# Performance work log

Measured on AMD Instinct MI355X. Metric: run time of the kernel, lower is better.

The kernel has to match this reference:

```python
import jax, jax.numpy as jnp
import numpy as np

N, E = 50000, 600000
IN_C, HID, OUT_C = 256, 128, 2
R, B, L = 7, 8, 3
ALPHA = 0.1


def _rgcn(x, src, dst, etype, comp, basis, root, bias):
    # comp: [R,B], basis: [B,d,d] -> per-relation weights W: [R,d,d]
    n, d = x.shape
    W = jnp.einsum('rb,bdf->rdf', comp, basis)
    # combined (dst, relation) segment id for per-relation mean aggregation
    seg = dst * R + etype
    msg = x[src]  # [E,d] gather
    s = jax.ops.segment_sum(msg, seg, num_segments=n * R)  # [N*R,d]
    cnt = jax.ops.segment_sum(jnp.ones((E,), x.dtype), seg, num_segments=n * R)
    agg = (s / jnp.maximum(cnt, 1.0)[:, None]).reshape(n, R, d)  # per-relation mean
    return x @ root + bias + jnp.einsum('nrd,rdf->nf', agg, W)


def setup_inputs() -> dict:
    key = jax.random.key(0)
    ks = jax.random.split(key, 10)
    sc = 0.05
    x = jax.random.normal(ks[0], (N, IN_C), dtype=jnp.float32)
    edge_index = jax.random.randint(ks[1], (2, E), 0, N)
    edge_type = jax.random.randint(ks[2], (E,), 0, R)
    # GPR temp init: alpha*(1-alpha)^k, last entry (1-alpha)^K
    temp = jnp.asarray(ALPHA * (1.0 - ALPHA) ** np.arange(L + 1), dtype=jnp.float32)
    temp = temp.at[-1].set((1.0 - ALPHA) ** L)
    lin1_w = jax.random.normal(ks[3], (IN_C, HID), jnp.float32) * sc
    lin1_b = jnp.zeros((HID,), jnp.float32)
    lin2_w = jax.random.normal(ks[4], (HID, OUT_C), jnp.float32) * sc
    lin2_b = jnp.zeros((OUT_C,), jnp.float32)
    comps = jax.random.normal(ks[5], (L, R, B), jnp.float32) * sc
    bases = jax.random.normal(ks[6], (L, B, HID, HID), jnp.float32) * sc
    roots = jax.random.normal(ks[7], (L, HID, HID), jnp.float32) * sc
    conv_biases = jnp.zeros((L, HID), jnp.float32)
    return dict(x=x, edge_index=edge_index, edge_type=edge_type, temp=temp,
                lin1_w=lin1_w, lin1_b=lin1_b, lin2_w=lin2_w, lin2_b=lin2_b,
                comps=comps, bases=bases, roots=roots, conv_biases=conv_biases)


def reference(x, edge_index, edge_type, temp, lin1_w, lin1_b, lin2_w, lin2_b,
              comps, bases, roots, conv_biases):
    src, dst = edge_index[0], edge_index[1]
    h = x @ lin1_w + lin1_b
    hidden = h * temp[0]
    cur = hidden
    for i in range(L):
        cur = _rgcn(cur, src, dst, edge_type, comps[i], bases[i], roots[i], conv_biases[i])
        if i < L - 1:
            cur = jax.nn.relu(cur)  # dropout p=0.4 is identity in eval mode
        hidden = hidden + temp[i + 1] * cur
    return hidden @ lin2_w + lin2_b
```

## Files before the change

### kernel.cpp

```cpp
#include <hip/hip_runtime.h>
#include <cstdint>


constexpr int N_NODES  = 50000;
constexpr int E_EDGES  = 600000;
constexpr int R_REL    = 7;
constexpr int HID      = 128;
constexpr int IN_C     = 256;
constexpr int L_LAYERS = 3;
constexpr int AGG_COLS = 896;
constexpr int K_CAT    = 1024;
constexpr int NR       = N_NODES * R_REL;
constexpr int SCANR_BLOCKS = (NR + 255) / 256;

#define DEVI __device__ __forceinline__

using short8  = __attribute__((ext_vector_type(8))) short;
using floatx4 = __attribute__((ext_vector_type(4))) float;

DEVI unsigned short f2bf(float f) {
  unsigned u = __float_as_uint(f);
  unsigned r = (u + 0x7FFFu + ((u >> 16) & 1u)) >> 16;
  return (unsigned short)r;
}
DEVI float bf2f(unsigned short h) { return __uint_as_float(((unsigned)h) << 16); }

__global__ __launch_bounds__(256) void cast_w1_kernel(
    const float* __restrict__ w1, unsigned short* __restrict__ w1T)
{
  int t = blockIdx.x * 256 + threadIdx.x;
  if (t >= HID * IN_C) return;
  int m = t >> 8, k = t & 255;
  w1T[m * IN_C + k] = f2bf(w1[k * HID + m]);
}

__global__ __launch_bounds__(256) void build_wcat2(
    const float* __restrict__ comps,
    const float* __restrict__ bases,
    const float* __restrict__ roots,
    unsigned short* __restrict__ wcat2T)
{
  int t = blockIdx.x * 256 + threadIdx.x;
  if (t >= L_LAYERS * 128 * K_CAT) return;
  int l   = t >> 17;
  int rem = t & 131071;
  int f   = rem >> 10;
  int k   = rem & 1023;
  float v;
  if (k < 128) {
    v = roots[((size_t)l * 128 + k) * 128 + f];
  } else {
    int r = (k - 128) >> 7, d = (k - 128) & 127;
    const float* cp = comps + ((size_t)l * R_REL + r) * 8;
    const float* bp = bases + (((size_t)l * 8) * 128 + d) * 128 + f;
    float s = 0.f;
#pragma unroll
    for (int b = 0; b < 8; ++b) s += cp[b] * bp[(size_t)b * 128 * 128];
    v = s;
  }
  wcat2T[t] = f2bf(v);
}

__global__ __launch_bounds__(256) void hist_kernel(
    const int* __restrict__ ei, const int* __restrict__ et,
    int* __restrict__ cntRel)
{
  int e = blockIdx.x * 256 + threadIdx.x;
  if (e >= E_EDGES) return;
  atomicAdd(&cntRel[ei[E_EDGES + e] * R_REL + et[e]], 1);
}

__global__ __launch_bounds__(256) void scanA_kernel(
    const int* __restrict__ cnt, int* __restrict__ tmpOff,
    int* __restrict__ blockSums)
{
  __shared__ int s[256];
  int i = blockIdx.x * 256 + threadIdx.x;
  int v = (i < NR) ? cnt[i] : 0;
  s[threadIdx.x] = v;
  __syncthreads();
#pragma unroll
  for (int d = 1; d < 256; d <<= 1) {
    int t = (threadIdx.x >= d) ? s[threadIdx.x - d] : 0;
    __syncthreads();
    s[threadIdx.x] += t;
    __syncthreads();
  }
  if (i < NR) tmpOff[i] = s[threadIdx.x] - v;
  if (threadIdx.x == 255) blockSums[blockIdx.x] = s[255];
}

__global__ __launch_bounds__(256) void scanB_kernel(int* __restrict__ bs)
{
  __shared__ int s[256];
  __shared__ int carry;
  if (threadIdx.x == 0) carry = 0;
  __syncthreads();
  for (int base = 0; base < SCANR_BLOCKS; base += 256) {
    int cOld = carry;
    int i = base + threadIdx.x;
    int v = (i < SCANR_BLOCKS) ? bs[i] : 0;
    s[threadIdx.x] = v;
    __syncthreads();
#pragma unroll
    for (int d = 1; d < 256; d <<= 1) {
      int t = (threadIdx.x >= d) ? s[threadIdx.x - d] : 0;
      __syncthreads();
      s[threadIdx.x] += t;
      __syncthreads();
    }
    if (i < SCANR_BLOCKS) bs[i] = s[threadIdx.x] - v + cOld;
    __syncthreads();
    if (threadIdx.x == 0) carry = cOld + s[255];
    __syncthreads();
  }
}

__global__ __launch_bounds__(256) void scanC_kernel(
    const int* __restrict__ tmpOff, const int* __restrict__ blockSums,
    int* __restrict__ drs)
{
  int i = blockIdx.x * 256 + threadIdx.x;
  if (i < NR) drs[i] = tmpOff[i] + blockSums[blockIdx.x];
  if (i == 0) drs[NR] = E_EDGES;
}

__global__ __launch_bounds__(256) void place_kernel(
    const int* __restrict__ ei, const int* __restrict__ et,
    const int* __restrict__ drs, int* __restrict__ cursor,
    unsigned short* __restrict__ esrc)
{
  int e = blockIdx.x * 256 + threadIdx.x;
  if (e >= E_EDGES) return;
  int seg = ei[E_EDGES + e] * R_REL + et[e];
  int pos = drs[seg] + atomicAdd(&cursor[seg], 1);
  esrc[pos] = (unsigned short)ei[e];
}

__global__ __launch_bounds__(256) void agg_reg_kernel(
    const unsigned short* __restrict__ curA,
    const unsigned short* __restrict__ esrc,
    const int* __restrict__ drs,
    unsigned short* __restrict__ aggB)
{
  const int tid  = threadIdx.x;
  const int lane = tid & 63;
  const int dst  = blockIdx.x * 4 + (tid >> 6);
  if (dst >= N_NODES) return;
  const int segBase = dst * R_REL;

  int bnd = drs[segBase + (lane & 7)];
  const int a0    = __shfl(bnd, 0);
  const int total = __shfl(bnd, 7) - a0;

  int pk = 0;
  if (lane < total) pk = (int)esrc[a0 + lane];

  const unsigned* colp = (const unsigned*)curA + lane;

  int p = a0;
  int aPrev = a0;
#pragma unroll
  for (int r = 0; r < R_REL; ++r) {
    int br = __shfl(bnd, r + 1);
    float sx = 0.f, sy = 0.f;
    for (; p < br; ++p) {
      int idx = p - a0;
      int src = (idx < 64) ? __shfl(pk, idx) : (int)esrc[p];
      unsigned v = colp[src * 64];
      sx += bf2f((unsigned short)(v & 0xFFFF));
      sy += bf2f((unsigned short)(v >> 16));
    }
    int c = br - aPrev;
    float sc = (c > 0) ? 1.0f / (float)c : 0.f;
    unsigned pck = (unsigned)f2bf(sx * sc) | ((unsigned)f2bf(sy * sc) << 16);
    *(unsigned*)(aggB + (size_t)dst * AGG_COLS + r * HID + lane * 2) = pck;
    aPrev = br;
  }
}

__global__ __launch_bounds__(256) void gemm_lin1(
    const float* __restrict__ x,
    const unsigned short* __restrict__ BT,
    const float* __restrict__ bias,
    const float* __restrict__ temp,
    unsigned short* __restrict__ b0out)
{
  __shared__ unsigned short Atile[64][136];
  __shared__ unsigned short Btile[128][136];
  const int tid  = threadIdx.x;
  const int row0 = blockIdx.x * 64;
  const int lane = tid & 63;
  const int wid  = tid >> 6;
  const int wrow = (wid & 1) * 32;
  const int wcol = (wid >> 1) * 64;
  const int l15  = lane & 15;
  const int quad = lane >> 4;

  floatx4 acc[2][4] = {};

  for (int k0 = 0; k0 < IN_C; k0 += 128) {
#pragma unroll
    for (int it = 0; it < 4; ++it) {
      int chunk = it * 256 + tid;
      int r = chunk >> 4, cc = (chunk & 15) << 3;
      int grow = row0 + r;
      uint4 va = make_uint4(0u, 0u, 0u, 0u);
      if (grow < N_NODES) {
        const float* xp = x + (size_t)grow * IN_C + k0 + cc;
        float4 f0 = *(const float4*)xp;
        float4 f1 = *(const float4*)(xp + 4);
        va.x = (unsigned)f2bf(f0.x) | ((unsigned)f2bf(f0.y) << 16);
        va.y = (unsigned)f2bf(f0.z) | ((unsigned)f2bf(f0.w) << 16);
        va.z = (unsigned)f2bf(f1.x) | ((unsigned)f2bf(f1.y) << 16);
        va.w = (unsigned)f2bf(f1.z) | ((unsigned)f2bf(f1.w) << 16);
      }
      *(uint4*)(&Atile[r][cc]) = va;
    }
#pragma unroll
    for (int it = 0; it < 8; ++it) {
      int chunk = it * 256 + tid;
      int n = chunk >> 4, cc = (chunk & 15) << 3;
      *(uint4*)(&Btile[n][cc]) =
          *(const uint4*)(BT + (size_t)n * IN_C + k0 + cc);
    }
    __syncthreads();
#pragma unroll
    for (int ks = 0; ks < 4; ++ks) {
      int kc = ks * 32 + quad * 8;
      short8 af[2], bfr[4];
#pragma unroll
      for (int i = 0; i < 2; ++i)
        af[i] = *(const short8*)(&Atile[wrow + i * 16 + l15][kc]);
#pragma unroll
      for (int j = 0; j < 4; ++j)
        bfr[j] = *(const short8*)(&Btile[wcol + j * 16 + l15][kc]);
#pragma unroll
      for (int i = 0; i < 2; ++i)
#pragma unroll
        for (int j = 0; j < 4; ++j)
          acc[i][j] = __builtin_amdgcn_mfma_f32_16x16x32_bf16(
              af[i], bfr[j], acc[i][j], 0, 0, 0);
    }
    __syncthreads();
  }

  float t0 = temp[0];
#pragma unroll
  for (int i = 0; i < 2; ++i) {
    int lrow0 = wrow + i * 16 + quad * 4;
#pragma unroll
    for (int j = 0; j < 4; ++j) {
      int gcol = wcol + j * 16 + l15;
      float bb = bias[gcol];
#pragma unroll
      for (int r = 0; r < 4; ++r)
        Atile[lrow0 + r][gcol] = f2bf(t0 * (acc[i][j][r] + bb));
    }
  }
  __syncthreads();
#pragma unroll
  for (int it = 0; it < 4; ++it) {
    int chunk = it * 256 + tid;
    int r = chunk >> 4, cc = (chunk & 15) << 3;
    int grow = row0 + r;
    if (grow < N_NODES)
      *(uint4*)(b0out + (size_t)grow * HID + cc) = *(const uint4*)(&Atile[r][cc]);
  }
}

__global__ __launch_bounds__(256) void gemm_layer(
    const unsigned short* __restrict__ curA,
    const unsigned short* __restrict__ aggB,
    const unsigned short* __restrict__ BT,
    const float* __restrict__ bias,
    unsigned short* __restrict__ bout,
    int layer)
{
  __shared__ unsigned short Atile[32][136];
  __shared__ unsigned short Btile[128][136];
  const int tid  = threadIdx.x;
  const int row0 = blockIdx.x * 32;
  const int lane = tid & 63;
  const int wid  = tid >> 6;
  const int wrow = (wid & 1) * 16;
  const int wcol = (wid >> 1) * 64;
  const int l15  = lane & 15;
  const int quad = lane >> 4;

  floatx4 acc[4] = {};

  for (int p = 0; p < 8; ++p) {
#pragma unroll
    for (int it = 0; it < 8; ++it) {
      int chunk = it * 256 + tid;
      int n = chunk >> 4, cc = (chunk & 15) << 3;
      *(uint4*)(&Btile[n][cc]) =
          *(const uint4*)(BT + (size_t)n * K_CAT + p * 128 + cc);
    }
#pragma unroll
    for (int it = 0; it < 2; ++it) {
      int chunk = it * 256 + tid;
      int r = chunk >> 4, cc = (chunk & 15) << 3;
      int grow = row0 + r;
      uint4 va = make_uint4(0u, 0u, 0u, 0u);
      if (grow < N_NODES) {
        if (p == 0)
          va = *(const uint4*)(curA + (size_t)grow * HID + cc);
        else
          va = *(const uint4*)(aggB + (size_t)grow * AGG_COLS +
                               (p - 1) * 128 + cc);
      }
      *(uint4*)(&Atile[r][cc]) = va;
    }
    __syncthreads();
#pragma unroll
    for (int ks = 0; ks < 4; ++ks) {
      int kc = ks * 32 + quad * 8;
      short8 af = *(const short8*)(&Atile[wrow + l15][kc]);
      short8 bfr[4];
#pragma unroll
      for (int j = 0; j < 4; ++j)
        bfr[j] = *(const short8*)(&Btile[wcol + j * 16 + l15][kc]);
#pragma unroll
      for (int j = 0; j < 4; ++j)
        acc[j] = __builtin_amdgcn_mfma_f32_16x16x32_bf16(af, bfr[j], acc[j],
                                                         0, 0, 0);
    }
    __syncthreads();
  }

  const bool isLast = (layer == L_LAYERS - 1);
  {
    int lrow0 = wrow + quad * 4;
#pragma unroll
    for (int j = 0; j < 4; ++j) {
      int gcol = wcol + j * 16 + l15;
      float bb = bias[gcol];
#pragma unroll
      for (int r = 0; r < 4; ++r) {
        float c = acc[j][r] + bb;
        if (!isLast) c = fmaxf(c, 0.f);
        Atile[lrow0 + r][gcol] = f2bf(c);
      }
    }
  }
  __syncthreads();
#pragma unroll
  for (int it = 0; it < 2; ++it) {
    int chunk = it * 256 + tid;
    int r = chunk >> 4, cc = (chunk & 15) << 3;
    int grow = row0 + r;
    if (grow < N_NODES)
      *(uint4*)(bout + (size_t)grow * HID + cc) = *(const uint4*)(&Atile[r][cc]);
  }
}

__global__ __launch_bounds__(256) void final_kernel(
    const unsigned short* __restrict__ b0, const unsigned short* __restrict__ b1,
    const unsigned short* __restrict__ b2v, const unsigned short* __restrict__ b3,
    const float* __restrict__ temp,
    const float* __restrict__ w2, const float* __restrict__ b2bias,
    float* __restrict__ out)
{
  int node = blockIdx.x * 4 + (threadIdx.x >> 6);
  int lane = threadIdx.x & 63;
  if (node >= N_NODES) return;
  float t1 = temp[1], t2 = temp[2], t3 = temp[3];
  size_t base = (size_t)node * 64 + lane;
  unsigned u0 = ((const unsigned*)b0)[base];
  unsigned u1 = ((const unsigned*)b1)[base];
  unsigned u2 = ((const unsigned*)b2v)[base];
  unsigned u3 = ((const unsigned*)b3)[base];
  float hx = bf2f((unsigned short)(u0 & 0xFFFF)) +
             t1 * bf2f((unsigned short)(u1 & 0xFFFF)) +
             t2 * bf2f((unsigned short)(u2 & 0xFFFF)) +
             t3 * bf2f((unsigned short)(u3 & 0xFFFF));
  float hy = bf2f((unsigned short)(u0 >> 16)) +
             t1 * bf2f((unsigned short)(u1 >> 16)) +
             t2 * bf2f((unsigned short)(u2 >> 16)) +
             t3 * bf2f((unsigned short)(u3 >> 16));
  int d0 = lane * 2, d1 = lane * 2 + 1;
  float a0 = hx * w2[d0 * 2 + 0] + hy * w2[d1 * 2 + 0];
  float a1 = hx * w2[d0 * 2 + 1] + hy * w2[d1 * 2 + 1];
#pragma unroll
  for (int off = 32; off > 0; off >>= 1) {
    a0 += __shfl_down(a0, off);
    a1 += __shfl_down(a1, off);
  }
  if (lane == 0) {
    out[node * 2 + 0] = a0 + b2bias[0];
    out[node * 2 + 1] = a1 + b2bias[1];
  }
}

extern "C" void kernel_launch(void* const* d_in, const int* in_sizes, int n_in,
                              void* d_out, int out_size, void* d_ws, size_t ws_size,
                              hipStream_t stream) {
  const float* x     = (const float*)d_in[0];
  const int*   ei    = (const int*)d_in[1];
  const int*   et    = (const int*)d_in[2];
  const float* temp  = (const float*)d_in[3];
  const float* w1    = (const float*)d_in[4];
  const float* b1    = (const float*)d_in[5];
  const float* w2    = (const float*)d_in[6];
  const float* b2    = (const float*)d_in[7];
  const float* comps = (const float*)d_in[8];
  const float* bases = (const float*)d_in[9];
  const float* roots = (const float*)d_in[10];
  const float* cbias = (const float*)d_in[11];

  char* ws = (char*)d_ws;
  size_t off = 0;
  auto take = [&](size_t bytes) {
    char* p = ws + off;
    off = (off + bytes + 255) & ~(size_t)255;
    return p;
  };
  unsigned short* wcat2T = (unsigned short*)take((size_t)L_LAYERS * 128 * K_CAT * 2);
  unsigned short* w1T    = (unsigned short*)take((size_t)HID * IN_C * 2);
  int*   cntRel  = (int*)take((size_t)NR * 4);
  int*   tmpOffR = (int*)take((size_t)NR * 4);
  int*   blockSumsR = (int*)take((size_t)SCANR_BLOCKS * 4);
  int*   drs     = (int*)take((size_t)(NR + 1) * 4);
  int*   cursorR = (int*)take((size_t)NR * 4);
  unsigned short* esrc = (unsigned short*)take((size_t)E_EDGES * 2);
  unsigned short* bl[L_LAYERS + 1];
  for (int i = 0; i <= L_LAYERS; ++i)
    bl[i] = (unsigned short*)take((size_t)N_NODES * HID * 2);
  unsigned short* aggB = (unsigned short*)take((size_t)N_NODES * AGG_COLS * 2);

  hipMemsetAsync(cntRel, 0, (size_t)NR * 4, stream);
  hipMemsetAsync(cursorR, 0, (size_t)NR * 4, stream);

  hipLaunchKernelGGL(build_wcat2, dim3((L_LAYERS * 128 * K_CAT + 255) / 256),
                     dim3(256), 0, stream, comps, bases, roots, wcat2T);
  hipLaunchKernelGGL(cast_w1_kernel, dim3((HID * IN_C + 255) / 256), dim3(256),
                     0, stream, w1, w1T);
  hipLaunchKernelGGL(hist_kernel, dim3((E_EDGES + 255) / 256), dim3(256), 0,
                     stream, ei, et, cntRel);
  hipLaunchKernelGGL(scanA_kernel, dim3(SCANR_BLOCKS), dim3(256), 0, stream,
                     cntRel, tmpOffR, blockSumsR);
  hipLaunchKernelGGL(scanB_kernel, dim3(1), dim3(256), 0, stream, blockSumsR);
  hipLaunchKernelGGL(scanC_kernel, dim3(SCANR_BLOCKS), dim3(256), 0, stream,
                     tmpOffR, blockSumsR, drs);
  hipLaunchKernelGGL(place_kernel, dim3((E_EDGES + 255) / 256), dim3(256), 0,
                     stream, ei, et, drs, cursorR, esrc);

  const int rowBlocks64 = (N_NODES + 63) / 64;
  const int rowBlocks32 = (N_NODES + 31) / 32;
  hipLaunchKernelGGL(gemm_lin1, dim3(rowBlocks64), dim3(256), 0, stream,
                     x, w1T, b1, temp, bl[0]);

  for (int l = 0; l < L_LAYERS; ++l) {
    hipLaunchKernelGGL(agg_reg_kernel, dim3((N_NODES + 3) / 4), dim3(256),
                       0, stream, bl[l], esrc, drs, aggB);
    hipLaunchKernelGGL(gemm_layer, dim3(rowBlocks32), dim3(256), 0, stream,
                       bl[l], aggB, wcat2T + (size_t)l * 128 * K_CAT,
                       cbias + (size_t)l * HID, bl[l + 1], l);
  }

  hipLaunchKernelGGL(final_kernel, dim3((N_NODES + 3) / 4), dim3(256), 0, stream,
                     bl[0], bl[1], bl[2], bl[3], temp, w2, b2, (float*)d_out);
}
```

Measured before the change: 525.0 us.

## Fuse per-relation mean aggregation into layer GEMM with double-buffered gather

Removes the separate aggregation kernel and its N×896 bf16 intermediate buffer. The layer GEMM now gathers neighbor rows per relation directly into a double-buffered LDS A-tile, issuing the next relation's loads while the current relation's MFMA runs. This saves the global write and re-read of the aggregated features and one kernel launch per layer. In exchange it raises register pressure (32-entry gather buffer, launch_bounds 256,3) and adds per-wave serial gather latency inside the GEMM.

```diff
diff --git a/kernel.cpp b/kernel.cpp
--- a/kernel.cpp
+++ b/kernel.cpp
@@ -8,7 +8,6 @@
 constexpr int HID      = 128;
 constexpr int IN_C     = 256;
 constexpr int L_LAYERS = 3;
-constexpr int AGG_COLS = 896;
 constexpr int K_CAT    = 1024;
 constexpr int NR       = N_NODES * R_REL;
 constexpr int SCANR_BLOCKS = (NR + 255) / 256;
@@ -135,48 +134,6 @@
   int seg = ei[E_EDGES + e] * R_REL + et[e];
   int pos = drs[seg] + atomicAdd(&cursor[seg], 1);
   esrc[pos] = (unsigned short)ei[e];
-}
-
-__global__ __launch_bounds__(256) void agg_reg_kernel(
-    const unsigned short* __restrict__ curA,
-    const unsigned short* __restrict__ esrc,
-    const int* __restrict__ drs,
-    unsigned short* __restrict__ aggB)
-{
-  const int tid  = threadIdx.x;
-  const int lane = tid & 63;
-  const int dst  = blockIdx.x * 4 + (tid >> 6);
-  if (dst >= N_NODES) return;
-  const int segBase = dst * R_REL;
-
-  int bnd = drs[segBase + (lane & 7)];
-  const int a0    = __shfl(bnd, 0);
-  const int total = __shfl(bnd, 7) - a0;
-
-  int pk = 0;
-  if (lane < total) pk = (int)esrc[a0 + lane];
-
-  const unsigned* colp = (const unsigned*)curA + lane;
-
-  int p = a0;
-  int aPrev = a0;
-#pragma unroll
-  for (int r = 0; r < R_REL; ++r) {
-    int br = __shfl(bnd, r + 1);
-    float sx = 0.f, sy = 0.f;
-    for (; p < br; ++p) {
-      int idx = p - a0;
-      int src = (idx < 64) ? __shfl(pk, idx) : (int)esrc[p];
-      unsigned v = colp[src * 64];
-      sx += bf2f((unsigned short)(v & 0xFFFF));
-      sy += bf2f((unsigned short)(v >> 16));
-    }
-    int c = br - aPrev;
-    float sc = (c > 0) ? 1.0f / (float)c : 0.f;
-    unsigned pck = (unsigned)f2bf(sx * sc) | ((unsigned)f2bf(sy * sc) << 16);
-    *(unsigned*)(aggB + (size_t)dst * AGG_COLS + r * HID + lane * 2) = pck;
-    aPrev = br;
-  }
 }
 
 __global__ __launch_bounds__(256) void gemm_lin1(
@@ -269,15 +226,16 @@
   }
 }
 
-__global__ __launch_bounds__(256) void gemm_layer(
+__global__ __launch_bounds__(256, 3) void gemm_layer(
     const unsigned short* __restrict__ curA,
-    const unsigned short* __restrict__ aggB,
+    const unsigned short* __restrict__ esrc,
+    const int* __restrict__ drs,
     const unsigned short* __restrict__ BT,
     const float* __restrict__ bias,
     unsigned short* __restrict__ bout,
     int layer)
 {
-  __shared__ unsigned short Atile[32][136];
+  __shared__ unsigned short Atile[2][32][136];
   __shared__ unsigned short Btile[128][136];
   const int tid  = threadIdx.x;
   const int row0 = blockIdx.x * 32;
@@ -288,7 +246,82 @@
   const int l15  = lane & 15;
   const int quad = lane >> 4;
 
+  const int d0 = row0 + wid * 8;
+  int bidx = d0 * R_REL + ((lane < 56) ? lane : 56);
+  if (bidx > NR) bidx = NR;
+  const int bv = drs[bidx];
+  const int A0     = __shfl(bv, 0);
+  const int totalW = __shfl(bv, 56) - A0;
+  int pk0 = 0, pk1 = 0;
+  if (lane < totalW)      pk0 = (int)esrc[A0 + lane];
+  if (64 + lane < totalW) pk1 = (int)esrc[A0 + 64 + lane];
+  const unsigned* colp = (const unsigned*)curA + lane;
+  unsigned rowv[32];
+
   floatx4 acc[4] = {};
+
+#pragma unroll
+  for (int it = 0; it < 2; ++it) {
+    int chunk = it * 256 + tid;
+    int r = chunk >> 4, cc = (chunk & 15) << 3;
+    int grow = row0 + r;
+    uint4 va = make_uint4(0u, 0u, 0u, 0u);
+    if (grow < N_NODES) va = *(const uint4*)(curA + (size_t)grow * HID + cc);
+    *(uint4*)(&Atile[0][r][cc]) = va;
+  }
+
+  auto selsrc = [&](int idx) -> int {
+    int uidx = __builtin_amdgcn_readfirstlane(idx);
+    if (uidx < 128) {
+      int pv = (uidx < 64) ? pk0 : pk1;
+      return __shfl(pv, uidx & 63);
+    }
+    return (int)esrc[A0 + uidx];
+  };
+
+  auto gissue = [&](int r) {
+#pragma unroll
+    for (int i = 0; i < 8; ++i) {
+      int a = __shfl(bv, i * 7 + r);
+      int b = __shfl(bv, i * 7 + r + 1);
+      int rc = __builtin_amdgcn_readfirstlane(b - a);
+      if (rc > 0) rowv[i * 4 + 0] = colp[(size_t)selsrc(a - A0) * 64];
+      if (rc > 1) rowv[i * 4 + 1] = colp[(size_t)selsrc(a + 1 - A0) * 64];
+      if (rc > 2) rowv[i * 4 + 2] = colp[(size_t)selsrc(a + 2 - A0) * 64];
+      if (rc > 3) rowv[i * 4 + 3] = colp[(size_t)selsrc(a + 3 - A0) * 64];
+    }
+  };
+
+  auto gfinish = [&](int r, int nb) {
+#pragma unroll
+    for (int i = 0; i < 8; ++i) {
+      int a = __shfl(bv, i * 7 + r);
+      int b = __shfl(bv, i * 7 + r + 1);
+      int c = b - a;
+      int rc = __builtin_amdgcn_readfirstlane(c);
+      float sx = 0.f, sy = 0.f;
+      if (rc > 0) { unsigned u = rowv[i * 4 + 0];
+        sx += __uint_as_float(u << 16); sy += __uint_as_float(u & 0xFFFF0000u); }
+      if (rc > 1) { unsigned u = rowv[i * 4 + 1];
+        sx += __uint_as_float(u << 16); sy += __uint_as_float(u & 0xFFFF0000u); }
+      if (rc > 2) { unsigned u = rowv[i * 4 + 2];
+        sx += __uint_as_float(u << 16); sy += __uint_as_float(u & 0xFFFF0000u); }
+      if (rc > 3) { unsigned u = rowv[i * 4 + 3];
+        sx += __uint_as_float(u << 16); sy += __uint_as_float(u & 0xFFFF0000u); }
+      if (rc > 4) {
+        for (int e = a + 4; e < b; ++e) {
+          unsigned u = colp[(size_t)selsrc(e - A0) * 64];
+          sx += __uint_as_float(u << 16); sy += __uint_as_float(u & 0xFFFF0000u);
+        }
+      }
+      float sc = (rc > 0) ? __builtin_amdgcn_rcpf((float)c) : 0.f;
+      unsigned pck = (unsigned)f2bf(sx * sc) | ((unsigned)f2bf(sy * sc) << 16);
+      *(unsigned*)(&Atile[nb][wid * 8 + i][lane * 2]) = pck;
+    }
+  };
+
+  gissue(0);
+  __syncthreads();
 
   for (int p = 0; p < 8; ++p) {
 #pragma unroll
@@ -298,26 +331,14 @@
       *(uint4*)(&Btile[n][cc]) =
           *(const uint4*)(BT + (size_t)n * K_CAT + p * 128 + cc);
     }
-#pragma unroll
-    for (int it = 0; it < 2; ++it) {
-      int chunk = it * 256 + tid;
-      int r = chunk >> 4, cc = (chunk & 15) << 3;
-      int grow = row0 + r;
-      uint4 va = make_uint4(0u, 0u, 0u, 0u);
-      if (grow < N_NODES) {
-        if (p == 0)
-          va = *(const uint4*)(curA + (size_t)grow * HID + cc);
-        else
-          va = *(const uint4*)(aggB + (size_t)grow * AGG_COLS +
-                               (p - 1) * 128 + cc);
-      }
-      *(uint4*)(&Atile[r][cc]) = va;
-    }
-    __syncthreads();
+    if (p < 7) gfinish(p, (p + 1) & 1);
+    if (p < 6) gissue(p + 1);
+    __syncthreads();
+    const unsigned short (*Ab)[136] = Atile[p & 1];
 #pragma unroll
     for (int ks = 0; ks < 4; ++ks) {
       int kc = ks * 32 + quad * 8;
-      short8 af = *(const short8*)(&Atile[wrow + l15][kc]);
+      short8 af = *(const short8*)(&Ab[wrow + l15][kc]);
       short8 bfr[4];
 #pragma unroll
       for (int j = 0; j < 4; ++j)
@@ -341,7 +362,7 @@
       for (int r = 0; r < 4; ++r) {
         float c = acc[j][r] + bb;
         if (!isLast) c = fmaxf(c, 0.f);
-        Atile[lrow0 + r][gcol] = f2bf(c);
+        Atile[0][lrow0 + r][gcol] = f2bf(c);
       }
     }
   }
@@ -352,7 +373,8 @@
     int r = chunk >> 4, cc = (chunk & 15) << 3;
     int grow = row0 + r;
     if (grow < N_NODES)
-      *(uint4*)(bout + (size_t)grow * HID + cc) = *(const uint4*)(&Atile[r][cc]);
+      *(uint4*)(bout + (size_t)grow * HID + cc) =
+          *(const uint4*)(&Atile[0][r][cc]);
   }
 }
 
@@ -428,7 +450,6 @@
   unsigned short* bl[L_LAYERS + 1];
   for (int i = 0; i <= L_LAYERS; ++i)
     bl[i] = (unsigned short*)take((size_t)N_NODES * HID * 2);
-  unsigned short* aggB = (unsigned short*)take((size_t)N_NODES * AGG_COLS * 2);
 
   hipMemsetAsync(cntRel, 0, (size_t)NR * 4, stream);
   hipMemsetAsync(cursorR, 0, (size_t)NR * 4, stream);
@@ -453,10 +474,8 @@
                      x, w1T, b1, temp, bl[0]);
 
   for (int l = 0; l < L_LAYERS; ++l) {
-    hipLaunchKernelGGL(agg_reg_kernel, dim3((N_NODES + 3) / 4), dim3(256),
-                       0, stream, bl[l], esrc, drs, aggB);
     hipLaunchKernelGGL(gemm_layer, dim3(rowBlocks32), dim3(256), 0, stream,
-                       bl[l], aggB, wcat2T + (size_t)l * 128 * K_CAT,
+                       bl[l], esrc, drs, wcat2T + (size_t)l * 128 * K_CAT,
                        cbias + (size_t)l * HID, bl[l + 1], l);
   }
 
```

Result: slower. 666.3 us (+26.9%).
